# Optimization experiments

Measured on AMD Instinct MI355X. Metric: run time of the kernel, lower is better.

The kernel has to match this reference:

```python
import jax, jax.numpy as jnp
import numpy as np

N, E, F_IN, H, G, C, L = 100000, 1600000, 128, 128, 1000, 10, 3
EPS = 1e-5


def setup_inputs() -> dict:
    key = jax.random.key(0)
    ks = jax.random.split(key, 10)
    x = jax.random.normal(ks[0], (N, F_IN), dtype=jnp.float32)
    edge_index = jax.random.randint(ks[1], (2, E), 0, N, dtype=jnp.int64)
    batch = jnp.sort(jax.random.randint(ks[2], (N,), 0, G, dtype=jnp.int64))
    s = 1.0 / np.sqrt(H)
    conv_w = jax.random.normal(ks[3], (L, F_IN, H), dtype=jnp.float32) * s
    conv_b = jnp.zeros((L, H), dtype=jnp.float32)
    bn_gamma = jnp.ones((L, H), dtype=jnp.float32)
    bn_beta = jnp.zeros((L, H), dtype=jnp.float32)
    w1 = jax.random.normal(ks[4], (H, H // 2), dtype=jnp.float32) * s
    b1 = jnp.zeros((H // 2,), dtype=jnp.float32)
    w2 = jax.random.normal(ks[5], (H // 2, C), dtype=jnp.float32) * (1.0 / np.sqrt(H // 2))
    b2 = jnp.zeros((C,), dtype=jnp.float32)
    return {"x": x, "conv_w": conv_w, "conv_b": conv_b, "bn_gamma": bn_gamma,
            "bn_beta": bn_beta, "w1": w1, "b1": b1, "w2": w2, "b2": b2,
            "edge_index": edge_index, "batch": batch}


def _gcn_conv(x, w, b, src, dst):
    # PyG GCNConv: h = x @ W; symmetric-normalized aggregation with self-loops.
    h = x @ w  # [N, H]
    deg = 1.0 + jax.ops.segment_sum(jnp.ones((E,), x.dtype), dst, num_segments=N)
    dinv = jax.lax.rsqrt(deg)  # [N]
    norm = dinv[src] * dinv[dst]  # [E]
    agg = jax.ops.segment_sum(h[src] * norm[:, None], dst, num_segments=N)
    agg = agg + h * (dinv * dinv)[:, None]  # self-loop contribution
    return agg + b


def _batchnorm(x, gamma, beta):
    mean = jnp.mean(x, axis=0)
    var = jnp.mean(jnp.square(x - mean), axis=0)  # biased, as in torch BN fwd
    return gamma * (x - mean) * jax.lax.rsqrt(var + EPS) + beta


def reference(x, conv_w, conv_b, bn_gamma, bn_beta, w1, b1, w2, b2, edge_index, batch):
    src, dst = edge_index[0], edge_index[1]
    h = x
    for i in range(L):
        h = _gcn_conv(h, conv_w[i], conv_b[i], src, dst)
        h = _batchnorm(h, bn_gamma[i], bn_beta[i])
        h = jax.nn.relu(h)  # dropout is identity in eval mode
    # global mean pool over graphs
    sums = jax.ops.segment_sum(h, batch, num_segments=G)
    cnts = jax.ops.segment_sum(jnp.ones((N,), h.dtype), batch, num_segments=G)
    pooled = sums / jnp.maximum(cnts, 1.0)[:, None]
    # classifier MLP
    z = jax.nn.relu(pooled @ w1 + b1)
    return z @ w2 + b2
```

## Files before the change

### kernel.cpp

```cpp
#include <hip/hip_runtime.h>
#include <hip/hip_bf16.h>

#define N_NODES 100000
#define N_EDGES 1600000
#define HDIM    128
#define NGRAPH  1000
#define NCLASS  10
#define BN_EPS  1e-5f

#define NBUCKET 391
#define TILE3   8192
#define GATHER_BLOCKS 1024

typedef short short8_t __attribute__((ext_vector_type(8)));
typedef float f32x4_t  __attribute__((ext_vector_type(4)));

__device__ __forceinline__ float bf2f(ushort u) {
    union { unsigned int i; float f; } v; v.i = ((unsigned int)u) << 16; return v.f;
}
__device__ __forceinline__ ushort f2bf(float f) {
    union { float f; unsigned int i; } v; v.f = f;
    unsigned int i = v.i;
    unsigned int r = i + 0x7fffu + ((i >> 16) & 1u);
    return (ushort)(r >> 16);
}
__device__ __forceinline__ float lo16(unsigned int u) {
    union { unsigned int i; float f; } v; v.i = u << 16; return v.f;
}
__device__ __forceinline__ float hi16(unsigned int u) {
    union { unsigned int i; float f; } v; v.i = u & 0xffff0000u; return v.f;
}

__global__ __launch_bounds__(256)
void bucket_hist(const int* __restrict__ dst, int* __restrict__ gcnt) {
    __shared__ int h[NBUCKET];
    int t = threadIdx.x;
    for (int i = t; i < NBUCKET; i += 256) h[i] = 0;
    __syncthreads();
    int i0 = blockIdx.x * blockDim.x + t;
    int stride = gridDim.x * blockDim.x;
    for (int e = i0; e < N_EDGES; e += stride)
        atomicAdd(&h[dst[e] >> 8], 1);
    __syncthreads();
    for (int i = t; i < NBUCKET; i += 256)
        if (h[i]) atomicAdd(&gcnt[i], h[i]);
}

__global__ void bucket_scan(const int* __restrict__ gcnt, int* __restrict__ bucket_base,
                            int* __restrict__ bucket_cursor, int* __restrict__ row_start) {
    if (threadIdx.x == 0) {
        int s = 0;
        for (int i = 0; i < NBUCKET; i++) {
            bucket_base[i] = s;
            bucket_cursor[i] = s;
            s += gcnt[i];
        }
        bucket_base[NBUCKET] = s;
        row_start[N_NODES] = N_EDGES;
    }
}

__global__ __launch_bounds__(256)
void scatter_pairs(const int* __restrict__ src, const int* __restrict__ dst,
                   int* __restrict__ bucket_cursor, unsigned int* __restrict__ pairs) {
    __shared__ int lhist[NBUCKET];
    __shared__ int lbase[NBUCKET];
    __shared__ int lcur[NBUCKET];
    int t = threadIdx.x;
    long tile0 = (long)blockIdx.x * TILE3;
    for (int i = t; i < NBUCKET; i += 256) { lhist[i] = 0; lcur[i] = 0; }
    __syncthreads();
    #pragma unroll 4
    for (int i = 0; i < TILE3 / 256; i++) {
        long e = tile0 + t + i * 256;
        if (e < N_EDGES) atomicAdd(&lhist[dst[e] >> 8], 1);
    }
    __syncthreads();
    for (int i = t; i < NBUCKET; i += 256)
        if (lhist[i] > 0) lbase[i] = atomicAdd(&bucket_cursor[i], lhist[i]);
    __syncthreads();
    #pragma unroll 4
    for (int i = 0; i < TILE3 / 256; i++) {
        long e = tile0 + t + i * 256;
        if (e < N_EDGES) {
            int d = dst[e];
            int bkt = d >> 8;
            int p = atomicAdd(&lcur[bkt], 1);
            pairs[lbase[bkt] + p] = (unsigned int)src[e] | ((unsigned int)(d & 255) << 24);
        }
    }
}

__global__ __launch_bounds__(256)
void build_csr(const unsigned int* __restrict__ pairs, const int* __restrict__ bucket_base,
               int* __restrict__ row_start, int* __restrict__ csr_src, float* __restrict__ dinv) {
    __shared__ int hist[256];
    __shared__ int cur[256];
    __shared__ int wsum[4];
    int b = blockIdx.x;
    int t = threadIdx.x;
    int beg = bucket_base[b], end = bucket_base[b + 1];
    hist[t] = 0;
    __syncthreads();
    for (int e = beg + t; e < end; e += 256)
        atomicAdd(&hist[pairs[e] >> 24], 1);
    __syncthreads();
    int v = hist[t];
    int lane = t & 63, wid = t >> 6;
    int x = v;
    #pragma unroll
    for (int off = 1; off < 64; off <<= 1) {
        int y = __shfl_up(x, off, 64);
        if (lane >= off) x += y;
    }
    if (lane == 63) wsum[wid] = x;
    __syncthreads();
    if (t == 0) {
        int s = 0;
        #pragma unroll
        for (int w = 0; w < 4; w++) { int tmp = wsum[w]; wsum[w] = s; s += tmp; }
    }
    __syncthreads();
    int excl = wsum[wid] + (x - v);
    cur[t] = excl;
    int node = b * 256 + t;
    if (node < N_NODES) {
        row_start[node] = beg + excl;
        dinv[node] = rsqrtf(1.0f + (float)v);
    }
    __syncthreads();
    for (int e = beg + t; e < end; e += 256) {
        unsigned int pk = pairs[e];
        int ln = pk >> 24;
        int sp = atomicAdd(&cur[ln], 1);
        csr_src[beg + sp] = (int)(pk & 0xFFFFFFu);
    }
}

__global__ __launch_bounds__(256)
void conv_w_prep(const float* __restrict__ W, ushort* __restrict__ wtbT) {
    int l = blockIdx.x >> 4, slice = blockIdx.x & 15;
    int t = threadIdx.x;
    int idx = slice * 1024 + t * 4;
    int k = idx >> 7, n = idx & 127;
    float4 w4 = *(const float4*)&W[(size_t)l * 16384 + k * 128 + n];
    ushort* o = wtbT + (size_t)l * 16384;
    o[(n + 0) * 128 + k] = f2bf(w4.x);
    o[(n + 1) * 128 + k] = f2bf(w4.y);
    o[(n + 2) * 128 + k] = f2bf(w4.z);
    o[(n + 3) * 128 + k] = f2bf(w4.w);
}

__global__ __launch_bounds__(256)
void gemm_mfma(const float* __restrict__ in, const ushort* __restrict__ wtbT,
               const float* __restrict__ bnp, const float* __restrict__ dinv,
               ushort* __restrict__ out) {
    __shared__ ushort as_[64][136];
    __shared__ ushort wt[128][136];
    int t = threadIdx.x;
    int wave = t >> 6, lane = t & 63;
    int g = lane >> 4, c = lane & 15;
    int rowbase = blockIdx.x * 64;

    #pragma unroll
    for (int i = 0; i < 8; i++) {
        int cid = t + i * 256;
        int n = cid >> 4, ko = (cid & 15) * 8;
        uint4 v = *(const uint4*)&wtbT[n * 128 + ko];
        *(uint4*)&wt[n][ko] = v;
    }
    #pragma unroll
    for (int i = 0; i < 8; i++) {
        int cid = t + i * 256;
        int r = cid >> 5, co = (cid & 31) * 4;
        int row = rowbase + r;
        ushort4 pk = make_ushort4(0, 0, 0, 0);
        if (row < N_NODES) {
            float4 v = *(const float4*)&in[(size_t)row * HDIM + co];
            if (bnp != nullptr) {
                float4 sc = *(const float4*)&bnp[co];
                float4 sh = *(const float4*)&bnp[128 + co];
                v.x = fmaxf(0.f, fmaf(v.x, sc.x, sh.x));
                v.y = fmaxf(0.f, fmaf(v.y, sc.y, sh.y));
                v.z = fmaxf(0.f, fmaf(v.z, sc.z, sh.z));
                v.w = fmaxf(0.f, fmaf(v.w, sc.w, sh.w));
            }
            pk.x = f2bf(v.x); pk.y = f2bf(v.y); pk.z = f2bf(v.z); pk.w = f2bf(v.w);
        }
        *(ushort4*)&as_[r][co] = pk;
    }
    __syncthreads();

    int m0 = wave * 16;
    short8_t a[4];
    #pragma unroll
    for (int ch = 0; ch < 4; ch++)
        a[ch] = *(const short8_t*)&as_[m0 + c][ch * 32 + g * 8];
    f32x4_t acc[8] = {};
    #pragma unroll
    for (int ct = 0; ct < 8; ct++) {
        #pragma unroll
        for (int ch = 0; ch < 4; ch++) {
            short8_t b = *(const short8_t*)&wt[ct * 16 + c][ch * 32 + g * 8];
            acc[ct] = __builtin_amdgcn_mfma_f32_16x16x32_bf16(a[ch], b, acc[ct], 0, 0, 0);
        }
    }
    float dv[4];
    #pragma unroll
    for (int reg = 0; reg < 4; reg++) {
        int rr = rowbase + m0 + g * 4 + reg;
        dv[reg] = dinv[rr < N_NODES ? rr : 0];
    }
    __syncthreads();
    #pragma unroll
    for (int ct = 0; ct < 8; ct++)
        #pragma unroll
        for (int reg = 0; reg < 4; reg++)
            as_[m0 + g * 4 + reg][ct * 16 + c] = f2bf(acc[ct][reg] * dv[reg]);
    __syncthreads();
    #pragma unroll
    for (int i = 0; i < 8; i++) {
        int cid = t + i * 256;
        int r = cid >> 5, co = (cid & 31) * 4;
        int row = rowbase + r;
        if (row < N_NODES)
            *(ushort4*)&out[(size_t)row * HDIM + co] = *(const ushort4*)&as_[r][co];
    }
}

__global__ __launch_bounds__(256)
void gather_agg(const ushort* __restrict__ hw, const int* __restrict__ row_start,
                const int* __restrict__ csr_src, const float* __restrict__ dinv,
                const float* __restrict__ bias, float* __restrict__ aggout,
                float* __restrict__ Spart, float* __restrict__ Qpart) {
    __shared__ float s_sum[128];
    __shared__ float s_sq[128];
    int t = threadIdx.x;
    if (t < 128) { s_sum[t] = 0.f; s_sq[t] = 0.f; }
    __syncthreads();
    int lane = t & 63, wid = t >> 6;
    int g = lane >> 4, c = lane & 15;
    int fo = c * 8;
    float4 bA = *(const float4*)&bias[fo];
    float4 bB = *(const float4*)&bias[fo + 4];
    float ls[8] = {}, lq[8] = {};
    int gw = blockIdx.x * 4 + wid;
    int nw = gridDim.x * 4;
    for (int n = gw; n < N_NODES; n += nw) {
        int jb = row_start[n], je = row_start[n + 1];
        float acc[8] = {};
        int j = jb;
        for (; j + 8 <= je; j += 8) {
            int sa = csr_src[j + 2 * g];
            int sb = csr_src[j + 2 * g + 1];
            uint4 p = *(const uint4*)&hw[(size_t)sa * HDIM + fo];
            uint4 q = *(const uint4*)&hw[(size_t)sb * HDIM + fo];
            acc[0] += lo16(p.x) + lo16(q.x);
            acc[1] += hi16(p.x) + hi16(q.x);
            acc[2] += lo16(p.y) + lo16(q.y);
            acc[3] += hi16(p.y) + hi16(q.y);
            acc[4] += lo16(p.z) + lo16(q.z);
            acc[5] += hi16(p.z) + hi16(q.z);
            acc[6] += lo16(p.w) + lo16(q.w);
            acc[7] += hi16(p.w) + hi16(q.w);
        }
        int e0 = j + g, e1 = j + 4 + g;
        if (e0 < je) {
            int s = csr_src[e0];
            uint4 p = *(const uint4*)&hw[(size_t)s * HDIM + fo];
            acc[0] += lo16(p.x); acc[1] += hi16(p.x);
            acc[2] += lo16(p.y); acc[3] += hi16(p.y);
            acc[4] += lo16(p.z); acc[5] += hi16(p.z);
            acc[6] += lo16(p.w); acc[7] += hi16(p.w);
        }
        if (e1 < je) {
            int s = csr_src[e1];
            uint4 p = *(const uint4*)&hw[(size_t)s * HDIM + fo];
            acc[0] += lo16(p.x); acc[1] += hi16(p.x);
            acc[2] += lo16(p.y); acc[3] += hi16(p.y);
            acc[4] += lo16(p.z); acc[5] += hi16(p.z);
            acc[6] += lo16(p.w); acc[7] += hi16(p.w);
        }
        #pragma unroll
        for (int i = 0; i < 8; i++) {
            acc[i] += __shfl_xor(acc[i], 16);
            acc[i] += __shfl_xor(acc[i], 32);
        }
        uint4 ps = *(const uint4*)&hw[(size_t)n * HDIM + fo];
        float dn = dinv[n];
        float r[8];
        r[0] = fmaf(acc[0] + lo16(ps.x), dn, bA.x);
        r[1] = fmaf(acc[1] + hi16(ps.x), dn, bA.y);
        r[2] = fmaf(acc[2] + lo16(ps.y), dn, bA.z);
        r[3] = fmaf(acc[3] + hi16(ps.y), dn, bA.w);
        r[4] = fmaf(acc[4] + lo16(ps.z), dn, bB.x);
        r[5] = fmaf(acc[5] + hi16(ps.z), dn, bB.y);
        r[6] = fmaf(acc[6] + lo16(ps.w), dn, bB.z);
        r[7] = fmaf(acc[7] + hi16(ps.w), dn, bB.w);
        if (g == 0) {
            *(float4*)&aggout[(size_t)n * HDIM + fo]     = make_float4(r[0], r[1], r[2], r[3]);
            *(float4*)&aggout[(size_t)n * HDIM + fo + 4] = make_float4(r[4], r[5], r[6], r[7]);
            #pragma unroll
            for (int i = 0; i < 8; i++) { ls[i] += r[i]; lq[i] += r[i] * r[i]; }
        }
    }
    if (g == 0) {
        #pragma unroll
        for (int i = 0; i < 8; i++) {
            atomicAdd(&s_sum[fo + i], ls[i]);
            atomicAdd(&s_sq[fo + i],  lq[i]);
        }
    }
    __syncthreads();
    if (t < 128) {
        Spart[(size_t)blockIdx.x * 128 + t] = s_sum[t];
        Qpart[(size_t)blockIdx.x * 128 + t] = s_sq[t];
    }
}

__global__ __launch_bounds__(256)
void bn_reduce_prep(const float* __restrict__ Spart, const float* __restrict__ Qpart,
                    const float* __restrict__ gamma, const float* __restrict__ beta,
                    float* __restrict__ bnp) {
    __shared__ float rs[32][8];
    __shared__ float rq[32][8];
    int t = threadIdx.x;
    int fi = t & 7, chunk = t >> 3;
    int f = blockIdx.x * 8 + fi;
    float s = 0.f, q = 0.f;
    for (int b = chunk; b < GATHER_BLOCKS; b += 32) {
        s += Spart[(size_t)b * 128 + f];
        q += Qpart[(size_t)b * 128 + f];
    }
    rs[chunk][fi] = s; rq[chunk][fi] = q;
    __syncthreads();
    if (t < 8) {
        float S = 0.f, Q = 0.f;
        #pragma unroll
        for (int cc = 0; cc < 32; cc++) { S += rs[cc][t]; Q += rq[cc][t]; }
        int ff = blockIdx.x * 8 + t;
        float mean = S * (1.0f / N_NODES);
        float var  = Q * (1.0f / N_NODES) - mean * mean;
        float inv  = rsqrtf(var + BN_EPS);
        float sc   = gamma[ff] * inv;
        bnp[ff]       = sc;
        bnp[128 + ff] = beta[ff] - mean * sc;
    }
}

__global__ __launch_bounds__(128)
void pool_kernel(const float* __restrict__ agg, const float* __restrict__ bnp,
                 const int* __restrict__ batch, float* __restrict__ pooled) {
    int g = blockIdx.x;
    int k = threadIdx.x;
    int lo = 0, hi = N_NODES;
    while (lo < hi) { int mid = (lo + hi) >> 1; if (batch[mid] < g) lo = mid + 1; else hi = mid; }
    int start = lo;
    hi = N_NODES;
    while (lo < hi) { int mid = (lo + hi) >> 1; if (batch[mid] < g + 1) lo = mid + 1; else hi = mid; }
    int end = lo;
    float sc = bnp[k], sh = bnp[128 + k];
    float sum = 0.f;
    for (int n = start; n < end; n++)
        sum += fmaxf(0.f, fmaf(agg[(size_t)n * HDIM + k], sc, sh));
    float cnt = (float)(end - start);
    pooled[g * HDIM + k] = sum / fmaxf(cnt, 1.0f);
}

__global__ __launch_bounds__(128)
void mlp_kernel(const float* __restrict__ pooled, const float* __restrict__ w1,
                const float* __restrict__ b1, const float* __restrict__ w2,
                const float* __restrict__ b2, float* __restrict__ out) {
    __shared__ float p[128];
    __shared__ float z[64];
    int g = blockIdx.x;
    int t = threadIdx.x;
    p[t] = pooled[g * HDIM + t];
    __syncthreads();
    if (t < 64) {
        float s = b1[t];
        #pragma unroll 8
        for (int k = 0; k < 128; k++) s += p[k] * w1[k * 64 + t];
        z[t] = fmaxf(0.f, s);
    }
    __syncthreads();
    if (t < NCLASS) {
        float s = b2[t];
        #pragma unroll
        for (int j = 0; j < 64; j++) s += z[j] * w2[j * NCLASS + t];
        out[g * NCLASS + t] = s;
    }
}

extern "C" void kernel_launch(void* const* d_in, const int* in_sizes, int n_in,
                              void* d_out, int out_size, void* d_ws, size_t ws_size,
                              hipStream_t stream) {
    const float* x      = (const float*)d_in[0];
    const float* conv_w = (const float*)d_in[1];
    const float* conv_b = (const float*)d_in[2];
    const float* gamma  = (const float*)d_in[3];
    const float* beta   = (const float*)d_in[4];
    const float* w1     = (const float*)d_in[5];
    const float* b1     = (const float*)d_in[6];
    const float* w2     = (const float*)d_in[7];
    const float* b2     = (const float*)d_in[8];
    const int*   ei     = (const int*)d_in[9];
    const int*   batch  = (const int*)d_in[10];
    float* out = (float*)d_out;

    char* ws = (char*)d_ws;
    size_t off = 0;
    auto alloc = [&](size_t bytes) -> void* {
        off = (off + 255) & ~(size_t)255;
        void* p = ws + off;
        off += bytes;
        return p;
    };
    ushort* A         = (ushort*)alloc((size_t)N_NODES * HDIM * 2);
    float*  B         = (float*) alloc((size_t)N_NODES * HDIM * 4);
    int*    csr_src   = (int*)   alloc((size_t)N_EDGES * 4);
    int*    row_start = (int*)   alloc((size_t)(N_NODES + 1) * 4);
    float*  dinv      = (float*) alloc((size_t)N_NODES * 4);
    int*    gcnt      = (int*)   alloc((size_t)NBUCKET * 4);
    int*    bbase     = (int*)   alloc((size_t)(NBUCKET + 1) * 4);
    int*    bcursor   = (int*)   alloc((size_t)NBUCKET * 4);
    ushort* wtbT      = (ushort*)alloc((size_t)3 * 16384 * 2);
    float*  Spart     = (float*) alloc((size_t)GATHER_BLOCKS * 128 * 4);
    float*  Qpart     = (float*) alloc((size_t)GATHER_BLOCKS * 128 * 4);
    float*  bnp       = (float*) alloc(3 * 256 * 4);
    float*  pooled    = (float*) alloc((size_t)NGRAPH * HDIM * 4);
    unsigned int* pairs = (unsigned int*)B;

    const int* srcv = ei;
    const int* dstv = ei + N_EDGES;

    hipMemsetAsync(gcnt, 0, (size_t)NBUCKET * 4, stream);

    bucket_hist  <<<256, 256, 0, stream>>>(dstv, gcnt);
    bucket_scan  <<<1, 64, 0, stream>>>(gcnt, bbase, bcursor, row_start);
    scatter_pairs<<<(N_EDGES + TILE3 - 1) / TILE3, 256, 0, stream>>>(srcv, dstv, bcursor, pairs);
    build_csr    <<<NBUCKET, 256, 0, stream>>>(pairs, bbase, row_start, csr_src, dinv);
    conv_w_prep  <<<48, 256, 0, stream>>>(conv_w, wtbT);

    for (int l = 0; l < 3; l++) {
        const float* inl  = (l == 0) ? x : B;
        const float* bnpl = (l == 0) ? nullptr : (bnp + (l - 1) * 256);
        gemm_mfma<<<(N_NODES + 63) / 64, 256, 0, stream>>>(inl, wtbT + (size_t)l * 16384,
                                                           bnpl, dinv, A);
        gather_agg<<<GATHER_BLOCKS, 256, 0, stream>>>(A, row_start, csr_src, dinv,
                                                      conv_b + l * HDIM, B, Spart, Qpart);
        bn_reduce_prep<<<16, 256, 0, stream>>>(Spart, Qpart, gamma + l * HDIM,
                                               beta + l * HDIM, bnp + l * 256);
    }
    pool_kernel<<<NGRAPH, 128, 0, stream>>>(B, bnp + 2 * 256, batch, pooled);
    mlp_kernel <<<NGRAPH, 128, 0, stream>>>(pooled, w1, b1, w2, b2, out);
}
```

Before: 582.0 us.

## Store aggregated activations in bf16, parallelize bucket scan, double gather blocks

The inter-layer aggregation buffer is stored as bf16 instead of fp32. This halves the bytes written by gather_agg and read by the next layer's GEMM and by pooling. The bucket prefix scan is parallelised with wave shuffles instead of running serially on one thread, and the gather grid grows from 1024 to 2048 blocks. BN statistics still come from fp32 values, but the normalised inputs now carry bf16 rounding error, and the larger grid means more partial sums for bn_reduce_prep to combine.

```diff
diff --git a/kernel.cpp b/kernel.cpp
--- a/kernel.cpp
+++ b/kernel.cpp
@@ -10,7 +10,7 @@
 
 #define NBUCKET 391
 #define TILE3   8192
-#define GATHER_BLOCKS 1024
+#define GATHER_BLOCKS 2048
 
 typedef short short8_t __attribute__((ext_vector_type(8)));
 typedef float f32x4_t  __attribute__((ext_vector_type(4)));
@@ -24,6 +24,9 @@
     unsigned int r = i + 0x7fffu + ((i >> 16) & 1u);
     return (ushort)(r >> 16);
 }
+__device__ __forceinline__ unsigned int pack2(float a, float b) {
+    return (unsigned int)f2bf(a) | ((unsigned int)f2bf(b) << 16);
+}
 __device__ __forceinline__ float lo16(unsigned int u) {
     union { unsigned int i; float f; } v; v.i = u << 16; return v.f;
 }
@@ -46,18 +49,29 @@
         if (h[i]) atomicAdd(&gcnt[i], h[i]);
 }
 
-__global__ void bucket_scan(const int* __restrict__ gcnt, int* __restrict__ bucket_base,
-                            int* __restrict__ bucket_cursor, int* __restrict__ row_start) {
-    if (threadIdx.x == 0) {
+__global__ __launch_bounds__(512)
+void bucket_scan(const int* __restrict__ gcnt, int* __restrict__ bucket_base,
+                 int* __restrict__ bucket_cursor, int* __restrict__ row_start) {
+    __shared__ int wsum[8];
+    int t = threadIdx.x, lane = t & 63, wid = t >> 6;
+    int v = (t < NBUCKET) ? gcnt[t] : 0;
+    int x = v;
+    #pragma unroll
+    for (int off = 1; off < 64; off <<= 1) {
+        int y = __shfl_up(x, off, 64);
+        if (lane >= off) x += y;
+    }
+    if (lane == 63) wsum[wid] = x;
+    __syncthreads();
+    if (t == 0) {
         int s = 0;
-        for (int i = 0; i < NBUCKET; i++) {
-            bucket_base[i] = s;
-            bucket_cursor[i] = s;
-            s += gcnt[i];
-        }
-        bucket_base[NBUCKET] = s;
-        row_start[N_NODES] = N_EDGES;
-    }
+        #pragma unroll
+        for (int w = 0; w < 8; w++) { int tmp = wsum[w]; wsum[w] = s; s += tmp; }
+    }
+    __syncthreads();
+    int excl = wsum[wid] + (x - v);
+    if (t < NBUCKET) { bucket_base[t] = excl; bucket_cursor[t] = excl; }
+    if (t == 0) { bucket_base[NBUCKET] = N_EDGES; row_start[N_NODES] = N_EDGES; }
 }
 
 __global__ __launch_bounds__(256)
@@ -152,9 +166,9 @@
 }
 
 __global__ __launch_bounds__(256)
-void gemm_mfma(const float* __restrict__ in, const ushort* __restrict__ wtbT,
-               const float* __restrict__ bnp, const float* __restrict__ dinv,
-               ushort* __restrict__ out) {
+void gemm_mfma(const float* __restrict__ inf, const ushort* __restrict__ inb,
+               const ushort* __restrict__ wtbT, const float* __restrict__ bnp,
+               const float* __restrict__ dinv, ushort* __restrict__ out) {
     __shared__ ushort as_[64][136];
     __shared__ ushort wt[128][136];
     int t = threadIdx.x;
@@ -169,25 +183,45 @@
         uint4 v = *(const uint4*)&wtbT[n * 128 + ko];
         *(uint4*)&wt[n][ko] = v;
     }
-    #pragma unroll
-    for (int i = 0; i < 8; i++) {
-        int cid = t + i * 256;
-        int r = cid >> 5, co = (cid & 31) * 4;
-        int row = rowbase + r;
-        ushort4 pk = make_ushort4(0, 0, 0, 0);
-        if (row < N_NODES) {
-            float4 v = *(const float4*)&in[(size_t)row * HDIM + co];
-            if (bnp != nullptr) {
-                float4 sc = *(const float4*)&bnp[co];
-                float4 sh = *(const float4*)&bnp[128 + co];
-                v.x = fmaxf(0.f, fmaf(v.x, sc.x, sh.x));
-                v.y = fmaxf(0.f, fmaf(v.y, sc.y, sh.y));
-                v.z = fmaxf(0.f, fmaf(v.z, sc.z, sh.z));
-                v.w = fmaxf(0.f, fmaf(v.w, sc.w, sh.w));
+    if (inf) {
+        #pragma unroll
+        for (int i = 0; i < 8; i++) {
+            int cid = t + i * 256;
+            int r = cid >> 5, co = (cid & 31) * 4;
+            int row = rowbase + r;
+            ushort4 pk = make_ushort4(0, 0, 0, 0);
+            if (row < N_NODES) {
+                float4 v = *(const float4*)&inf[(size_t)row * HDIM + co];
+                pk.x = f2bf(v.x); pk.y = f2bf(v.y); pk.z = f2bf(v.z); pk.w = f2bf(v.w);
             }
-            pk.x = f2bf(v.x); pk.y = f2bf(v.y); pk.z = f2bf(v.z); pk.w = f2bf(v.w);
-        }
-        *(ushort4*)&as_[r][co] = pk;
+            *(ushort4*)&as_[r][co] = pk;
+        }
+    } else {
+        #pragma unroll
+        for (int i = 0; i < 4; i++) {
+            int cid = t + i * 256;
+            int r = cid >> 4, co = (cid & 15) * 8;
+            int row = rowbase + r;
+            uint4 o = make_uint4(0, 0, 0, 0);
+            if (row < N_NODES) {
+                uint4 p = *(const uint4*)&inb[(size_t)row * HDIM + co];
+                float4 scA = *(const float4*)&bnp[co];
+                float4 scB = *(const float4*)&bnp[co + 4];
+                float4 shA = *(const float4*)&bnp[128 + co];
+                float4 shB = *(const float4*)&bnp[132 + co];
+                float v0 = fmaxf(0.f, fmaf(lo16(p.x), scA.x, shA.x));
+                float v1 = fmaxf(0.f, fmaf(hi16(p.x), scA.y, shA.y));
+                float v2 = fmaxf(0.f, fmaf(lo16(p.y), scA.z, shA.z));
+                float v3 = fmaxf(0.f, fmaf(hi16(p.y), scA.w, shA.w));
+                float v4 = fmaxf(0.f, fmaf(lo16(p.z), scB.x, shB.x));
+                float v5 = fmaxf(0.f, fmaf(hi16(p.z), scB.y, shB.y));
+                float v6 = fmaxf(0.f, fmaf(lo16(p.w), scB.z, shB.z));
+                float v7 = fmaxf(0.f, fmaf(hi16(p.w), scB.w, shB.w));
+                o.x = pack2(v0, v1); o.y = pack2(v2, v3);
+                o.z = pack2(v4, v5); o.w = pack2(v6, v7);
+            }
+            *(uint4*)&as_[r][co] = o;
+        }
     }
     __syncthreads();
 
@@ -231,7 +265,7 @@
 __global__ __launch_bounds__(256)
 void gather_agg(const ushort* __restrict__ hw, const int* __restrict__ row_start,
                 const int* __restrict__ csr_src, const float* __restrict__ dinv,
-                const float* __restrict__ bias, float* __restrict__ aggout,
+                const float* __restrict__ bias, ushort* __restrict__ aggout,
                 float* __restrict__ Spart, float* __restrict__ Qpart) {
     __shared__ float s_sum[128];
     __shared__ float s_sq[128];
@@ -298,8 +332,10 @@
         r[6] = fmaf(acc[6] + lo16(ps.w), dn, bB.z);
         r[7] = fmaf(acc[7] + hi16(ps.w), dn, bB.w);
         if (g == 0) {
-            *(float4*)&aggout[(size_t)n * HDIM + fo]     = make_float4(r[0], r[1], r[2], r[3]);
-            *(float4*)&aggout[(size_t)n * HDIM + fo + 4] = make_float4(r[4], r[5], r[6], r[7]);
+            uint4 o;
+            o.x = pack2(r[0], r[1]); o.y = pack2(r[2], r[3]);
+            o.z = pack2(r[4], r[5]); o.w = pack2(r[6], r[7]);
+            *(uint4*)&aggout[(size_t)n * HDIM + fo] = o;
             #pragma unroll
             for (int i = 0; i < 8; i++) { ls[i] += r[i]; lq[i] += r[i] * r[i]; }
         }
@@ -349,7 +385,7 @@
 }
 
 __global__ __launch_bounds__(128)
-void pool_kernel(const float* __restrict__ agg, const float* __restrict__ bnp,
+void pool_kernel(const ushort* __restrict__ agg, const float* __restrict__ bnp,
                  const int* __restrict__ batch, float* __restrict__ pooled) {
     int g = blockIdx.x;
     int k = threadIdx.x;
@@ -361,8 +397,19 @@
     int end = lo;
     float sc = bnp[k], sh = bnp[128 + k];
     float sum = 0.f;
-    for (int n = start; n < end; n++)
-        sum += fmaxf(0.f, fmaf(agg[(size_t)n * HDIM + k], sc, sh));
+    int n = start;
+    for (; n + 4 <= end; n += 4) {
+        float a0 = bf2f(agg[(size_t)(n + 0) * HDIM + k]);
+        float a1 = bf2f(agg[(size_t)(n + 1) * HDIM + k]);
+        float a2 = bf2f(agg[(size_t)(n + 2) * HDIM + k]);
+        float a3 = bf2f(agg[(size_t)(n + 3) * HDIM + k]);
+        sum += fmaxf(0.f, fmaf(a0, sc, sh));
+        sum += fmaxf(0.f, fmaf(a1, sc, sh));
+        sum += fmaxf(0.f, fmaf(a2, sc, sh));
+        sum += fmaxf(0.f, fmaf(a3, sc, sh));
+    }
+    for (; n < end; n++)
+        sum += fmaxf(0.f, fmaf(bf2f(agg[(size_t)n * HDIM + k]), sc, sh));
     float cnt = (float)(end - start);
     pooled[g * HDIM + k] = sum / fmaxf(cnt, 1.0f);
 }
@@ -417,7 +464,7 @@
         return p;
     };
     ushort* A         = (ushort*)alloc((size_t)N_NODES * HDIM * 2);
-    float*  B         = (float*) alloc((size_t)N_NODES * HDIM * 4);
+    ushort* aggB      = (ushort*)alloc((size_t)N_NODES * HDIM * 2);
     int*    csr_src   = (int*)   alloc((size_t)N_EDGES * 4);
     int*    row_start = (int*)   alloc((size_t)(N_NODES + 1) * 4);
     float*  dinv      = (float*) alloc((size_t)N_NODES * 4);
@@ -429,7 +476,7 @@
     float*  Qpart     = (float*) alloc((size_t)GATHER_BLOCKS * 128 * 4);
     float*  bnp       = (float*) alloc(3 * 256 * 4);
     float*  pooled    = (float*) alloc((size_t)NGRAPH * HDIM * 4);
-    unsigned int* pairs = (unsigned int*)B;
+    unsigned int* pairs = (unsigned int*)aggB;
 
     const int* srcv = ei;
     const int* dstv = ei + N_EDGES;
@@ -437,21 +484,21 @@
     hipMemsetAsync(gcnt, 0, (size_t)NBUCKET * 4, stream);
 
     bucket_hist  <<<256, 256, 0, stream>>>(dstv, gcnt);
-    bucket_scan  <<<1, 64, 0, stream>>>(gcnt, bbase, bcursor, row_start);
+    bucket_scan  <<<1, 512, 0, stream>>>(gcnt, bbase, bcursor, row_start);
     scatter_pairs<<<(N_EDGES + TILE3 - 1) / TILE3, 256, 0, stream>>>(srcv, dstv, bcursor, pairs);
     build_csr    <<<NBUCKET, 256, 0, stream>>>(pairs, bbase, row_start, csr_src, dinv);
     conv_w_prep  <<<48, 256, 0, stream>>>(conv_w, wtbT);
 
     for (int l = 0; l < 3; l++) {
-        const float* inl  = (l == 0) ? x : B;
-        const float* bnpl = (l == 0) ? nullptr : (bnp + (l - 1) * 256);
-        gemm_mfma<<<(N_NODES + 63) / 64, 256, 0, stream>>>(inl, wtbT + (size_t)l * 16384,
-                                                           bnpl, dinv, A);
+        gemm_mfma<<<(N_NODES + 63) / 64, 256, 0, stream>>>(
+            (l == 0) ? x : nullptr, (l == 0) ? nullptr : aggB,
+            wtbT + (size_t)l * 16384,
+            (l == 0) ? nullptr : (bnp + (l - 1) * 256), dinv, A);
         gather_agg<<<GATHER_BLOCKS, 256, 0, stream>>>(A, row_start, csr_src, dinv,
-                                                      conv_b + l * HDIM, B, Spart, Qpart);
+                                                      conv_b + l * HDIM, aggB, Spart, Qpart);
         bn_reduce_prep<<<16, 256, 0, stream>>>(Spart, Qpart, gamma + l * HDIM,
                                                beta + l * HDIM, bnp + l * 256);
     }
-    pool_kernel<<<NGRAPH, 128, 0, stream>>>(B, bnp + 2 * 256, batch, pooled);
+    pool_kernel<<<NGRAPH, 128, 0, stream>>>(aggB, bnp + 2 * 256, batch, pooled);
     mlp_kernel <<<NGRAPH, 128, 0, stream>>>(pooled, w1, b1, w2, b2, out);
 }
```

New measurement: 589.0 us. About the same (+1.2%).
